# Performance work log

Measured on AMD Instinct MI355X. Metric: run time of the kernel, lower is better.

Reference implementation:

```python
import jax, jax.numpy as jnp
import numpy as np

N = 50000   # nodes
E = 800000  # edges (before self-loops)
IN = 128    # input feature dim
H = 4       # attention heads


def setup_inputs() -> dict:
    key = jax.random.key(0)
    ks = jax.random.split(key, 32)
    f = lambda k, s: (jax.random.normal(k, s, dtype=jnp.float32) * 0.1)
    inp = {
        "x": jax.random.normal(ks[0], (N, IN), dtype=jnp.float32),
        "edge_index": jax.random.randint(ks[1], (2, E), 0, N, dtype=jnp.int32),
        "edge_attr": jax.random.normal(ks[2], (E, 1), dtype=jnp.float32),
        # GATConv 1: 128 -> 8 per head, 4 heads (concat -> 32)
        "W1": f(ks[3], (IN, 32)), "as1": f(ks[4], (H, 8)), "ad1": f(ks[5], (H, 8)), "b1": jnp.zeros((32,), jnp.float32),
        # GATConv 2: 32 -> 16 per head (concat -> 64)
        "W2": f(ks[6], (32, 64)), "as2": f(ks[7], (H, 16)), "ad2": f(ks[8], (H, 16)), "b2": jnp.zeros((64,), jnp.float32),
        # GATConv 3: 64 -> 32 per head (concat -> 128)
        "W3": f(ks[9], (64, 128)), "as3": f(ks[10], (H, 32)), "ad3": f(ks[11], (H, 32)), "b3": jnp.zeros((128,), jnp.float32),
        # GATConv 4: 128 -> 64 per head (concat -> 256)
        "W4": f(ks[12], (128, 256)), "as4": f(ks[13], (H, 64)), "ad4": f(ks[14], (H, 64)), "b4": jnp.zeros((256,), jnp.float32),
        # MLP head
        "Wr": f(ks[15], (256, 32)), "br": jnp.zeros((32,), jnp.float32),
        "Wf1": f(ks[16], (32, 64)), "bf1": jnp.zeros((64,), jnp.float32),
        "Wf2": f(ks[17], (64, 1)), "bf2": jnp.zeros((1,), jnp.float32),
    }
    return inp


def _gat_layer(x, W, a_src, a_dst, bias, src, dst):
    """PyG GATConv (concat=True, negative_slope=0.2, self-loops appended upstream)."""
    heads, C = a_src.shape
    h = (x @ W).reshape(-1, heads, C)              # [N, H, C]
    alpha_s = jnp.sum(h * a_src[None], axis=-1)    # [N, H]
    alpha_d = jnp.sum(h * a_dst[None], axis=-1)    # [N, H]
    e = jax.nn.leaky_relu(alpha_s[src] + alpha_d[dst], 0.2)  # [E', H]
    # segment softmax over incoming edges of each destination node
    emax = jax.ops.segment_max(e, dst, num_segments=N)
    ee = jnp.exp(e - emax[dst])
    denom = jax.ops.segment_sum(ee, dst, num_segments=N)
    alpha = ee / denom[dst]                        # [E', H]
    msg = h[src] * alpha[:, :, None]               # [E', H, C]
    out = jax.ops.segment_sum(msg, dst, num_segments=N)  # [N, H, C]
    return out.reshape(-1, heads * C) + bias


def reference(x, edge_index, edge_attr,
              W1, as1, ad1, b1, W2, as2, ad2, b2,
              W3, as3, ad3, b3, W4, as4, ad4, b4,
              Wr, br, Wf1, bf1, Wf2, bf2):
    # edge_attr is accepted but unused, matching the original forward.
    loop = jnp.arange(N, dtype=edge_index.dtype)
    src = jnp.concatenate([edge_index[0], loop])   # add self-loops (PyG default)
    dst = jnp.concatenate([edge_index[1], loop])
    h = jax.nn.elu(_gat_layer(x, W1, as1, ad1, b1, src, dst))
    h = jax.nn.elu(_gat_layer(h, W2, as2, ad2, b2, src, dst))
    h = jax.nn.elu(_gat_layer(h, W3, as3, ad3, b3, src, dst))
    h = jax.nn.elu(_gat_layer(h, W4, as4, ad4, b4, src, dst))
    h = jax.nn.elu(h @ Wr + br)
    h = jax.nn.elu(h @ Wf1 + bf1)
    return h @ Wf2 + bf2                           # [N, 1]
```

## Files before the change

kernel.cpp:

```cpp
#include <hip/hip_runtime.h>
#include <hip/hip_fp16.h>
#include <math.h>

constexpr int NN = 50000;
constexpr int NE = 800000;
constexpr int NEP = NE + NN;
constexpr int CAP = 96;
constexpr int SCAT_B = (NE / 8 + 255) / 256;
constexpr int PACK_B = 26;
constexpr int NT = (NN + 63) / 64;

typedef _Float16 half8_t __attribute__((ext_vector_type(8)));
typedef float    f32x4_t __attribute__((ext_vector_type(4)));
typedef unsigned int u32x4 __attribute__((ext_vector_type(4)));

__device__ __forceinline__ float lrelu02(float x) { return x > 0.f ? x : 0.2f * x; }
__device__ __forceinline__ float eluf(float x)    { return x > 0.f ? x : (__expf(x) - 1.f); }
__device__ __forceinline__ float pick4(float4 q, int hd) {
  return (hd == 0) ? q.x : (hd == 1) ? q.y : (hd == 2) ? q.z : q.w;
}

#define FMAMIX_LO(accv, pv, uv) \
  asm("v_fma_mix_f32 %0, %1, %2, %0 op_sel:[0,0,0] op_sel_hi:[0,1,0]" \
      : "+v"(accv) : "v"(pv), "v"(uv))
#define FMAMIX_HI(accv, pv, uv) \
  asm("v_fma_mix_f32 %0, %1, %2, %0 op_sel:[0,1,0] op_sel_hi:[0,1,0]" \
      : "+v"(accv) : "v"(pv), "v"(uv))


__device__ __forceinline__ void pack_w_one(const float* __restrict__ W,
                                           __half* __restrict__ Wp,
                                           int M, int tid, int total) {
  if (tid >= total) return;
  int CT = M >> 4;
  int l = tid & 63;
  int c = (tid >> 6) % CT;
  int kc = (tid >> 6) / CT;
  int n = l & 15, q = l >> 4;
  __half* dst = Wp + (size_t)tid * 8;
  const float* src = W + (size_t)(kc * 32 + q * 8) * M + c * 16 + n;
  #pragma unroll
  for (int j = 0; j < 8; j++) dst[j] = __float2half_rn(src[j * M]);
}


template<int M, int C, int CT>
__device__ __forceinline__ void alpha_epilogue(const f32x4_t* acc,
    const float* __restrict__ a_src, const float* __restrict__ a_dst,
    int row_base, int m, float* __restrict__ as_out, float* __restrict__ ad_out) {
  float aS[CT], aD[CT];
  #pragma unroll
  for (int c = 0; c < CT; c++) { aS[c] = a_src[c * 16 + m]; aD[c] = a_dst[c * 16 + m]; }

  if constexpr (C == 8) {
    #pragma unroll
    for (int r = 0; r < 4; r++) {
      float p0 = acc[0][r] * aS[0], p1 = acc[1][r] * aS[1];
      float q0 = acc[0][r] * aD[0], q1 = acc[1][r] * aD[1];
      #pragma unroll
      for (int off = 1; off < 8; off <<= 1) {
        p0 += __shfl_xor(p0, off); p1 += __shfl_xor(p1, off);
        q0 += __shfl_xor(q0, off); q1 += __shfl_xor(q1, off);
      }
      int row = row_base + r;
      if ((m & 7) == 0 && row < NN) {
        int hb = m >> 3;
        as_out[row * 4 + hb]     = p0;
        as_out[row * 4 + 2 + hb] = p1;
        ad_out[row * 4 + hb]     = q0;
        ad_out[row * 4 + 2 + hb] = q1;
      }
    }
  } else {
    constexpr int FPH = C / 16;
    #pragma unroll
    for (int r = 0; r < 4; r++) {
      float bs[4] = {0.f, 0.f, 0.f, 0.f}, bd[4] = {0.f, 0.f, 0.f, 0.f};
      #pragma unroll
      for (int c = 0; c < CT; c++) {
        int hd = c / FPH;
        bs[hd] += acc[c][r] * aS[c];
        bd[hd] += acc[c][r] * aD[c];
      }
      #pragma unroll
      for (int off = 1; off < 16; off <<= 1)
        #pragma unroll
        for (int h = 0; h < 4; h++) {
          bs[h] += __shfl_xor(bs[h], off);
          bd[h] += __shfl_xor(bd[h], off);
        }
      int row = row_base + r;
      if (m < 4 && row < NN) {
        float vs = (m == 0) ? bs[0] : (m == 1) ? bs[1] : (m == 2) ? bs[2] : bs[3];
        float vd = (m == 0) ? bd[0] : (m == 1) ? bd[1] : (m == 2) ? bd[2] : bd[3];
        as_out[row * 4 + m] = vs;
        ad_out[row * 4 + m] = vd;
      }
    }
  }
}


__global__ __launch_bounds__(256) void front_kernel(
    const int* __restrict__ edge_src, const int* __restrict__ edge_dst,
    int* __restrict__ count, int* __restrict__ csr_src,
    const float* __restrict__ W1,
    const float* __restrict__ W2, __half* __restrict__ Wp2,
    const float* __restrict__ W3, __half* __restrict__ Wp3,
    const float* __restrict__ W4, __half* __restrict__ Wp4,
    const float* __restrict__ Wr, __half* __restrict__ Wrp,
    const float* __restrict__ Wf1, __half* __restrict__ Wf1p,
    const float* __restrict__ x, __half* __restrict__ Ch,
    const float* __restrict__ a_src, const float* __restrict__ a_dst,
    float* __restrict__ as_out, float* __restrict__ ad_out) {
  int b = blockIdx.x;
  if (b >= NT) {
    int b2 = b - NT;
    if (b2 < SCAT_B) {
      int e0 = (b2 * 256 + threadIdx.x) * 8;
      if (e0 < NE) {
        int4 sa = *(const int4*)(edge_src + e0);
        int4 sb = *(const int4*)(edge_src + e0 + 4);
        int4 da = *(const int4*)(edge_dst + e0);
        int4 db = *(const int4*)(edge_dst + e0 + 4);
        int p0 = atomicAdd(&count[da.x], 1);
        int p1 = atomicAdd(&count[da.y], 1);
        int p2 = atomicAdd(&count[da.z], 1);
        int p3 = atomicAdd(&count[da.w], 1);
        int p4 = atomicAdd(&count[db.x], 1);
        int p5 = atomicAdd(&count[db.y], 1);
        int p6 = atomicAdd(&count[db.z], 1);
        int p7 = atomicAdd(&count[db.w], 1);
        if (p0 < CAP - 1) csr_src[da.x * CAP + p0] = sa.x;
        if (p1 < CAP - 1) csr_src[da.y * CAP + p1] = sa.y;
        if (p2 < CAP - 1) csr_src[da.z * CAP + p2] = sa.z;
        if (p3 < CAP - 1) csr_src[da.w * CAP + p3] = sa.w;
        if (p4 < CAP - 1) csr_src[db.x * CAP + p4] = sb.x;
        if (p5 < CAP - 1) csr_src[db.y * CAP + p5] = sb.y;
        if (p6 < CAP - 1) csr_src[db.z * CAP + p6] = sb.z;
        if (p7 < CAP - 1) csr_src[db.w * CAP + p7] = sb.w;
      }
      return;
    }
    int tid = (b2 - SCAT_B) * 256 + threadIdx.x;
    if (tid < 256)            pack_w_one(W2, Wp2, 64,  tid,        256);
    else if (tid < 1280)      pack_w_one(W3, Wp3, 128, tid - 256,  1024);
    else if (tid < 5376)      pack_w_one(W4, Wp4, 256, tid - 1280, 4096);
    else if (tid < 6400)      pack_w_one(Wr, Wrp, 32,  tid - 5376, 1024);
    else if (tid < 6656)      pack_w_one(Wf1, Wf1p, 64, tid - 6400, 256);
    return;
  }

  constexpr int M = 32, K = 128, CT = 2, KC = 4;
  __shared__ _Float16 Ah[64 * 40];
  __shared__ _Float16 Bs[KC * CT * 64 * 8];
  int t = threadIdx.x;
  int w = t >> 6, l = t & 63;
  int m = l & 15, q = l >> 4;
  int row0 = b * 64;

  #pragma unroll
  for (int u0 = 0; u0 < 2; u0++) {
    int u = t + u0 * 256;
    int ul = u & 63;
    int uc = (u >> 6) & 1;
    int ukc = u >> 7;
    int un = ul & 15, uq = ul >> 4;
    const float* src = W1 + (size_t)(ukc * 32 + uq * 8) * M + uc * 16 + un;
    _Float16* dst = &Bs[u * 8];
    #pragma unroll
    for (int j = 0; j < 8; j++) dst[j] = (_Float16)src[j * M];
  }

  f32x4_t acc[CT];
  #pragma unroll
  for (int c = 0; c < CT; c++) acc[c] = (f32x4_t){0.f, 0.f, 0.f, 0.f};

  for (int kc = 0; kc < KC; kc++) {
    __syncthreads();
    #pragma unroll
    for (int i = 0; i < 2; i++) {
      int idx = t + 256 * i;
      int row = idx >> 3, c4 = idx & 7;
      int gr = row0 + row; if (gr >= NN) gr = NN - 1;
      float4 v = *(const float4*)(x + (size_t)gr * K + kc * 32 + c4 * 4);
      _Float16 h4[4] = {(_Float16)v.x, (_Float16)v.y, (_Float16)v.z, (_Float16)v.w};
      *(uint2*)(&Ah[row * 40 + c4 * 4]) = *(const uint2*)h4;
    }
    __syncthreads();
    half8_t a = *(const half8_t*)(&Ah[(w * 16 + m) * 40 + q * 8]);
    #pragma unroll
    for (int c = 0; c < CT; c++) {
      half8_t bf = *(const half8_t*)(&Bs[((kc * CT + c) * 64 + l) * 8]);
      acc[c] = __builtin_amdgcn_mfma_f32_16x16x32_f16(a, bf, acc[c], 0, 0, 0);
    }
  }

  #pragma unroll
  for (int r = 0; r < 4; r++) {
    int row = row0 + w * 16 + q * 4 + r;
    if (row < NN) {
      #pragma unroll
      for (int c = 0; c < CT; c++)
        Ch[(size_t)row * M + c * 16 + m] = __float2half_rn(acc[c][r]);
    }
  }
  alpha_epilogue<M, 8, CT>(acc, a_src, a_dst, row0 + w * 16 + q * 4, m, as_out, ad_out);
}


template<int M, int K, int C>
__global__ __launch_bounds__(256) void gemm_mfma_f16_kernel(const __half* __restrict__ A,
    const __half* __restrict__ Wp, __half* __restrict__ Ch,
    const float* __restrict__ a_src, const float* __restrict__ a_dst,
    float* __restrict__ as_out, float* __restrict__ ad_out) {
  constexpr int CT = M / 16;
  constexpr int KC = K / 32;
  __shared__ _Float16 Ah[64 * 40];
  int t = threadIdx.x;
  int w = t >> 6, l = t & 63;
  int m = l & 15, q = l >> 4;
  int row0 = blockIdx.x * 64;

  f32x4_t acc[CT];
  #pragma unroll
  for (int c = 0; c < CT; c++) acc[c] = (f32x4_t){0.f, 0.f, 0.f, 0.f};

  const half8_t* Bfrag = (const half8_t*)Wp;

  for (int kc = 0; kc < KC; kc++) {
    __syncthreads();
    {
      int row = t >> 2, c8 = t & 3;
      int gr = row0 + row; if (gr >= NN) gr = NN - 1;
      uint4 v = *(const uint4*)(A + (size_t)gr * K + kc * 32 + c8 * 8);
      *(uint4*)(&Ah[row * 40 + c8 * 8]) = v;
    }
    __syncthreads();
    half8_t a = *(const half8_t*)(&Ah[(w * 16 + m) * 40 + q * 8]);
    #pragma unroll
    for (int c = 0; c < CT; c++) {
      half8_t b = Bfrag[(kc * CT + c) * 64 + l];
      acc[c] = __builtin_amdgcn_mfma_f32_16x16x32_f16(a, b, acc[c], 0, 0, 0);
    }
  }

  #pragma unroll
  for (int r = 0; r < 4; r++) {
    int row = row0 + w * 16 + q * 4 + r;
    if (row < NN) {
      #pragma unroll
      for (int c = 0; c < CT; c++)
        Ch[(size_t)row * M + c * 16 + m] = __float2half_rn(acc[c][r]);
    }
  }
  alpha_epilogue<M, C, CT>(acc, a_src, a_dst, row0 + w * 16 + q * 4, m, as_out, ad_out);
}


template<int HC, int C>
__global__ __launch_bounds__(256) void agg_kernel(const __half* __restrict__ h,
    const float* __restrict__ as_v, const float* __restrict__ ad_v,
    const int* __restrict__ count, const int* __restrict__ csr_src,
    const float* __restrict__ bias, __half* __restrict__ out) {
  constexpr int V = HC / 8;
  constexpr int G = 64 / V;
  constexpr int D = (HC >= 128) ? 6 : 4;
  __shared__ float4 see4[4][CAP];
  __shared__ int    ssrc[4][CAP];
  int wid = threadIdx.x >> 6, lane = threadIdx.x & 63;
  int dst = blockIdx.x * 4 + wid;
  int base = dst * CAP;
  int degE = count[dst]; if (degE > CAP - 1) degE = CAP - 1;
  int deg = degE + 1;
  float4 ad = *(const float4*)(ad_v + dst * 4);

  float d0 = 0.f, d1 = 0.f, d2 = 0.f, d3 = 0.f;
  #pragma unroll
  for (int it = 0; it < 2; it++) {
    int j = lane + it * 64;
    if (j < deg) {
      int s = (j == 0) ? dst : csr_src[base + j - 1];
      float4 as = *(const float4*)(as_v + s * 4);
      float4 x = make_float4(__expf(lrelu02(as.x + ad.x)), __expf(lrelu02(as.y + ad.y)),
                             __expf(lrelu02(as.z + ad.z)), __expf(lrelu02(as.w + ad.w)));
      ssrc[wid][j] = s; see4[wid][j] = x;
      d0 += x.x; d1 += x.y; d2 += x.z; d3 += x.w;
    }
  }
  #pragma unroll
  for (int off = 32; off > 0; off >>= 1) {
    d0 += __shfl_xor(d0, off); d1 += __shfl_xor(d1, off);
    d2 += __shfl_xor(d2, off); d3 += __shfl_xor(d3, off);
  }
  float4 inv = make_float4(1.f / d0, 1.f / d1, 1.f / d2, 1.f / d3);

  int g = lane / V, v = lane % V;
  int hd = (v * 8) / C;
  float invh = pick4(inv, hd);
  int steps = (deg + G - 1) / G;
  const char* hb = (const char*)h;

  float px[D];
  u32x4 hv[D];

  #define STAGE(kk, jexpr) { \
    int jj = (jexpr) * G + g; \
    bool okk = jj < deg; \
    int jc = okk ? jj : 0; \
    int s = ssrc[wid][jc]; \
    float xx = ((const float*)&see4[wid][jc])[hd]; \
    px[kk] = okk ? xx * invh : 0.f; \
    const void* ap = hb + (size_t)s * (HC * 2) + v * 16; \
    asm volatile("global_load_dwordx4 %0, %1, off" : "=v"(hv[kk]) : "v"(ap) : "memory"); \
  }

  #pragma unroll
  for (int k = 0; k < D; k++) STAGE(k, k)

  float acc[8];
  #pragma unroll
  for (int i = 0; i < 8; i++) acc[i] = 0.f;
  int nB = (steps + D - 1) / D;
  for (int b = 1; b <= nB; b++) {
    #pragma unroll
    for (int k = 0; k < D; k++) {
      if constexpr (D == 6) asm volatile("s_waitcnt vmcnt(5)" ::: "memory");
      else                  asm volatile("s_waitcnt vmcnt(3)" ::: "memory");
      __builtin_amdgcn_sched_barrier(0);
      u32x4 u = hv[k];
      float p = px[k];
      FMAMIX_LO(acc[0], p, u[0]); FMAMIX_HI(acc[1], p, u[0]);
      FMAMIX_LO(acc[2], p, u[1]); FMAMIX_HI(acc[3], p, u[1]);
      FMAMIX_LO(acc[4], p, u[2]); FMAMIX_HI(acc[5], p, u[2]);
      FMAMIX_LO(acc[6], p, u[3]); FMAMIX_HI(acc[7], p, u[3]);
      STAGE(k, b * D + k)
    }
  }
  asm volatile("s_waitcnt vmcnt(0)" ::: "memory");
  __builtin_amdgcn_sched_barrier(0);
  #undef STAGE

  #pragma unroll
  for (int off = V; off < 64; off <<= 1)
    #pragma unroll
    for (int i = 0; i < 8; i++) acc[i] += __shfl_xor(acc[i], off);

  if (lane < V) {
    const float4* b4 = (const float4*)bias;
    float4 ba = b4[2 * v], bb = b4[2 * v + 1];
    _Float16 o[8];
    o[0] = (_Float16)eluf(acc[0] + ba.x); o[1] = (_Float16)eluf(acc[1] + ba.y);
    o[2] = (_Float16)eluf(acc[2] + ba.z); o[3] = (_Float16)eluf(acc[3] + ba.w);
    o[4] = (_Float16)eluf(acc[4] + bb.x); o[5] = (_Float16)eluf(acc[5] + bb.y);
    o[6] = (_Float16)eluf(acc[6] + bb.z); o[7] = (_Float16)eluf(acc[7] + bb.w);
    *(uint4*)(out + (size_t)dst * HC + v * 8) = *(const uint4*)o;
  }
}


__global__ __launch_bounds__(256) void mlp_mfma_kernel(const __half* __restrict__ h4,
    const __half* __restrict__ Wrp, const float* __restrict__ br,
    const __half* __restrict__ Wf1p, const float* __restrict__ bf1,
    const float* __restrict__ Wf2, const float* __restrict__ bf2,
    float* __restrict__ out) {
  __shared__ _Float16 rS[64 * 40];
  int t = threadIdx.x;
  int w = t >> 6, l = t & 63;
  int m = l & 15, q = l >> 4;
  int row0 = blockIdx.x * 64;
  const half8_t* Bwr  = (const half8_t*)Wrp;
  const half8_t* Bwf1 = (const half8_t*)Wf1p;

  int arow = row0 + w * 16 + m; if (arow >= NN) arow = NN - 1;
  const half8_t* Arow = (const half8_t*)(h4 + (size_t)arow * 256);
  half8_t afr[8];
  #pragma unroll
  for (int kc = 0; kc < 8; kc++) afr[kc] = Arow[kc * 4 + q];
  f32x4_t acc1[2];
  acc1[0] = (f32x4_t){0.f, 0.f, 0.f, 0.f};
  acc1[1] = (f32x4_t){0.f, 0.f, 0.f, 0.f};
  #pragma unroll
  for (int kc = 0; kc < 8; kc++) {
    acc1[0] = __builtin_amdgcn_mfma_f32_16x16x32_f16(afr[kc], Bwr[(kc * 2 + 0) * 64 + l], acc1[0], 0, 0, 0);
    acc1[1] = __builtin_amdgcn_mfma_f32_16x16x32_f16(afr[kc], Bwr[(kc * 2 + 1) * 64 + l], acc1[1], 0, 0, 0);
  }
  #pragma unroll
  for (int c = 0; c < 2; c++)
    #pragma unroll
    for (int r = 0; r < 4; r++) {
      float vv = eluf(acc1[c][r] + br[c * 16 + m]);
      rS[(w * 16 + q * 4 + r) * 40 + c * 16 + m] = (_Float16)vv;
    }
  __syncthreads();

  half8_t a2 = *(const half8_t*)(&rS[(w * 16 + m) * 40 + q * 8]);
  f32x4_t acc2[4];
  #pragma unroll
  for (int c = 0; c < 4; c++) acc2[c] = (f32x4_t){0.f, 0.f, 0.f, 0.f};
  #pragma unroll
  for (int c = 0; c < 4; c++)
    acc2[c] = __builtin_amdgcn_mfma_f32_16x16x32_f16(a2, Bwf1[c * 64 + l], acc2[c], 0, 0, 0);

  float wv[4] = {Wf2[m], Wf2[16 + m], Wf2[32 + m], Wf2[48 + m]};
  float rsum[4];
  #pragma unroll
  for (int r = 0; r < 4; r++) {
    float sr = 0.f;
    #pragma unroll
    for (int c = 0; c < 4; c++)
      sr += eluf(acc2[c][r] + bf1[c * 16 + m]) * wv[c];
    #pragma unroll
    for (int off = 1; off < 16; off <<= 1) sr += __shfl_xor(sr, off);
    rsum[r] = sr;
  }
  if (m == 0) {
    float b = bf2[0];
    #pragma unroll
    for (int r = 0; r < 4; r++) {
      int row = row0 + w * 16 + q * 4 + r;
      if (row < NN) out[row] = rsum[r] + b;
    }
  }
}


extern "C" void kernel_launch(void* const* d_in, const int* in_sizes, int n_in,
                              void* d_out, int out_size, void* d_ws, size_t ws_size,
                              hipStream_t stream) {
  const float* x   = (const float*)d_in[0];
  const int*   ei  = (const int*)d_in[1];
  const float* W1  = (const float*)d_in[3];
  const float* as1 = (const float*)d_in[4];
  const float* ad1 = (const float*)d_in[5];
  const float* b1  = (const float*)d_in[6];
  const float* W2  = (const float*)d_in[7];
  const float* as2 = (const float*)d_in[8];
  const float* ad2 = (const float*)d_in[9];
  const float* b2  = (const float*)d_in[10];
  const float* W3  = (const float*)d_in[11];
  const float* as3 = (const float*)d_in[12];
  const float* ad3 = (const float*)d_in[13];
  const float* b3  = (const float*)d_in[14];
  const float* W4  = (const float*)d_in[15];
  const float* as4 = (const float*)d_in[16];
  const float* ad4 = (const float*)d_in[17];
  const float* b4  = (const float*)d_in[18];
  const float* Wr  = (const float*)d_in[19];
  const float* br  = (const float*)d_in[20];
  const float* Wf1 = (const float*)d_in[21];
  const float* bf1 = (const float*)d_in[22];
  const float* Wf2 = (const float*)d_in[23];
  const float* bf2 = (const float*)d_in[24];
  float* out = (float*)d_out;

  char* p = (char*)d_ws;
  auto alloc = [&](size_t bytes) {
    char* q = p;
    p += (bytes + 255) & ~(size_t)255;
    return q;
  };
  int* count   = (int*)alloc((size_t)NN * 4);
  int* csr_src = (int*)alloc((size_t)NN * CAP * 4);
  __half* Hh = (__half*)alloc((size_t)NN * 256 * 2);
  __half* B2 = (__half*)alloc((size_t)NN * 128 * 2);
  __half* B3 = (__half*)alloc((size_t)NN * 256 * 2);
  float* as_buf = (float*)alloc((size_t)NN * 4 * 4);
  float* ad_buf = (float*)alloc((size_t)NN * 4 * 4);
  __half* Wp2 = (__half*)alloc((size_t)32 * 64 * 2);
  __half* Wp3 = (__half*)alloc((size_t)64 * 128 * 2);
  __half* Wp4 = (__half*)alloc((size_t)128 * 256 * 2);
  __half* Wrp = (__half*)alloc((size_t)256 * 32 * 2);
  __half* Wf1p = (__half*)alloc((size_t)32 * 64 * 2);

  const int* edge_src = ei;
  const int* edge_dst = ei + NE;

  hipMemsetAsync(count, 0, (size_t)NN * 4, stream);
  front_kernel<<<NT + SCAT_B + PACK_B, 256, 0, stream>>>(
      edge_src, edge_dst, count, csr_src,
      W1, W2, Wp2, W3, Wp3, W4, Wp4, Wr, Wrp, Wf1, Wf1p,
      x, Hh, as1, ad1, as_buf, ad_buf);

  int gb  = NT;
  int ggb = NN / 4;

  agg_kernel<32, 8><<<ggb, 256, 0, stream>>>(Hh, as_buf, ad_buf, count, csr_src, b1, B2);

  gemm_mfma_f16_kernel<64, 32, 16><<<gb, 256, 0, stream>>>(B2, Wp2, Hh, as2, ad2, as_buf, ad_buf);
  agg_kernel<64, 16><<<ggb, 256, 0, stream>>>(Hh, as_buf, ad_buf, count, csr_src, b2, B3);

  gemm_mfma_f16_kernel<128, 64, 32><<<gb, 256, 0, stream>>>(B3, Wp3, Hh, as3, ad3, as_buf, ad_buf);
  agg_kernel<128, 32><<<ggb, 256, 0, stream>>>(Hh, as_buf, ad_buf, count, csr_src, b3, B2);

  gemm_mfma_f16_kernel<256, 128, 64><<<gb, 256, 0, stream>>>(B2, Wp4, Hh, as4, ad4, as_buf, ad_buf);
  agg_kernel<256, 64><<<ggb, 256, 0, stream>>>(Hh, as_buf, ad_buf, count, csr_src, b4, B3);

  mlp_mfma_kernel<<<gb, 256, 0, stream>>>(B3, Wrp, br, Wf1p, bf1, Wf2, bf2, out);
}
```

Before: 381.6 us.

## Fuse GAT aggregation with next layer's GEMM and attention epilogue

Layers 1-3 now use one fused kernel per layer. Each 512-thread block aggregates 64 destination nodes (8 per wave), keeps the ELU'd result in shared memory, then multiplies it by the next weight matrix with MFMA and computes the next layer's attention coefficients. This removes the global write and reload of the intermediate activations and three kernel launches. The cost is fewer blocks (782 instead of 12500), each with serial per-wave work, so occupancy and load balance for the latency-bound gather may suffer. Ping-pong buffers are added for the features and attention scores.

```diff
diff --git a/kernel.cpp b/kernel.cpp
--- a/kernel.cpp
+++ b/kernel.cpp
@@ -4,10 +4,8 @@
 
 constexpr int NN = 50000;
 constexpr int NE = 800000;
-constexpr int NEP = NE + NN;
 constexpr int CAP = 96;
 constexpr int SCAT_B = (NE / 8 + 255) / 256;
-constexpr int PACK_B = 26;
 constexpr int NT = (NN + 63) / 64;
 
 typedef _Float16 half8_t __attribute__((ext_vector_type(8)));
@@ -26,6 +24,17 @@
 #define FMAMIX_HI(accv, pv, uv) \
   asm("v_fma_mix_f32 %0, %1, %2, %0 op_sel:[0,1,0] op_sel_hi:[0,1,0]" \
       : "+v"(accv) : "v"(pv), "v"(uv))
+
+#define STAGE_G(kk, jexpr, STRIDE) { \
+    int jj = (jexpr) * G + g; \
+    bool okk = jj < deg; \
+    int jc = okk ? jj : 0; \
+    int s = ssrc[wid][jc]; \
+    float xx = ((const float*)&see4[wid][jc])[hd]; \
+    px[kk] = okk ? xx * invh : 0.f; \
+    const void* ap = hb + (size_t)s * (STRIDE) + v * 16; \
+    asm volatile("global_load_dwordx4 %0, %1, off" : "=v"(hv[kk]) : "v"(ap) : "memory"); \
+  }
 
 
 __device__ __forceinline__ void pack_w_one(const float* __restrict__ W,
@@ -44,58 +53,28 @@
 }
 
 
-template<int M, int C, int CT>
-__device__ __forceinline__ void alpha_epilogue(const f32x4_t* acc,
+__device__ __forceinline__ void alpha_epilogue8(const f32x4_t* acc,
     const float* __restrict__ a_src, const float* __restrict__ a_dst,
     int row_base, int m, float* __restrict__ as_out, float* __restrict__ ad_out) {
-  float aS[CT], aD[CT];
-  #pragma unroll
-  for (int c = 0; c < CT; c++) { aS[c] = a_src[c * 16 + m]; aD[c] = a_dst[c * 16 + m]; }
-
-  if constexpr (C == 8) {
-    #pragma unroll
-    for (int r = 0; r < 4; r++) {
-      float p0 = acc[0][r] * aS[0], p1 = acc[1][r] * aS[1];
-      float q0 = acc[0][r] * aD[0], q1 = acc[1][r] * aD[1];
-      #pragma unroll
-      for (int off = 1; off < 8; off <<= 1) {
-        p0 += __shfl_xor(p0, off); p1 += __shfl_xor(p1, off);
-        q0 += __shfl_xor(q0, off); q1 += __shfl_xor(q1, off);
-      }
-      int row = row_base + r;
-      if ((m & 7) == 0 && row < NN) {
-        int hb = m >> 3;
-        as_out[row * 4 + hb]     = p0;
-        as_out[row * 4 + 2 + hb] = p1;
-        ad_out[row * 4 + hb]     = q0;
-        ad_out[row * 4 + 2 + hb] = q1;
-      }
-    }
-  } else {
-    constexpr int FPH = C / 16;
-    #pragma unroll
-    for (int r = 0; r < 4; r++) {
-      float bs[4] = {0.f, 0.f, 0.f, 0.f}, bd[4] = {0.f, 0.f, 0.f, 0.f};
-      #pragma unroll
-      for (int c = 0; c < CT; c++) {
-        int hd = c / FPH;
-        bs[hd] += acc[c][r] * aS[c];
-        bd[hd] += acc[c][r] * aD[c];
-      }
-      #pragma unroll
-      for (int off = 1; off < 16; off <<= 1)
-        #pragma unroll
-        for (int h = 0; h < 4; h++) {
-          bs[h] += __shfl_xor(bs[h], off);
-          bd[h] += __shfl_xor(bd[h], off);
-        }
-      int row = row_base + r;
-      if (m < 4 && row < NN) {
-        float vs = (m == 0) ? bs[0] : (m == 1) ? bs[1] : (m == 2) ? bs[2] : bs[3];
-        float vd = (m == 0) ? bd[0] : (m == 1) ? bd[1] : (m == 2) ? bd[2] : bd[3];
-        as_out[row * 4 + m] = vs;
-        ad_out[row * 4 + m] = vd;
-      }
+  float aS[2], aD[2];
+  #pragma unroll
+  for (int c = 0; c < 2; c++) { aS[c] = a_src[c * 16 + m]; aD[c] = a_dst[c * 16 + m]; }
+  #pragma unroll
+  for (int r = 0; r < 4; r++) {
+    float p0 = acc[0][r] * aS[0], p1 = acc[1][r] * aS[1];
+    float q0 = acc[0][r] * aD[0], q1 = acc[1][r] * aD[1];
+    #pragma unroll
+    for (int off = 1; off < 8; off <<= 1) {
+      p0 += __shfl_xor(p0, off); p1 += __shfl_xor(p1, off);
+      q0 += __shfl_xor(q0, off); q1 += __shfl_xor(q1, off);
+    }
+    int row = row_base + r;
+    if ((m & 7) == 0 && row < NN) {
+      int hb2 = m >> 3;
+      as_out[row * 4 + hb2]     = p0;
+      as_out[row * 4 + 2 + hb2] = p1;
+      ad_out[row * 4 + hb2]     = q0;
+      ad_out[row * 4 + 2 + hb2] = q1;
     }
   }
 }
@@ -183,8 +162,8 @@
       int idx = t + 256 * i;
       int row = idx >> 3, c4 = idx & 7;
       int gr = row0 + row; if (gr >= NN) gr = NN - 1;
-      float4 v = *(const float4*)(x + (size_t)gr * K + kc * 32 + c4 * 4);
-      _Float16 h4[4] = {(_Float16)v.x, (_Float16)v.y, (_Float16)v.z, (_Float16)v.w};
+      float4 vv = *(const float4*)(x + (size_t)gr * K + kc * 32 + c4 * 4);
+      _Float16 h4[4] = {(_Float16)vv.x, (_Float16)vv.y, (_Float16)vv.z, (_Float16)vv.w};
       *(uint2*)(&Ah[row * 40 + c4 * 4]) = *(const uint2*)h4;
     }
     __syncthreads();
@@ -205,56 +184,172 @@
         Ch[(size_t)row * M + c * 16 + m] = __float2half_rn(acc[c][r]);
     }
   }
-  alpha_epilogue<M, 8, CT>(acc, a_src, a_dst, row0 + w * 16 + q * 4, m, as_out, ad_out);
-}
-
-
-template<int M, int K, int C>
-__global__ __launch_bounds__(256) void gemm_mfma_f16_kernel(const __half* __restrict__ A,
-    const __half* __restrict__ Wp, __half* __restrict__ Ch,
-    const float* __restrict__ a_src, const float* __restrict__ a_dst,
+  alpha_epilogue8(acc, a_src, a_dst, row0 + w * 16 + q * 4, m, as_out, ad_out);
+}
+
+
+template<int MK, int KK, int CC>
+__global__ __launch_bounds__(512) void fused_agg_gemm_kernel(
+    const __half* __restrict__ hin,
+    const float* __restrict__ as_v, const float* __restrict__ ad_v,
+    const int* __restrict__ count, const int* __restrict__ csr_src,
+    const float* __restrict__ bias,
+    const __half* __restrict__ Wp,
+    __half* __restrict__ hout,
+    const float* __restrict__ a_src2, const float* __restrict__ a_dst2,
     float* __restrict__ as_out, float* __restrict__ ad_out) {
-  constexpr int CT = M / 16;
-  constexpr int KC = K / 32;
-  __shared__ _Float16 Ah[64 * 40];
+  constexpr int V = KK / 8;
+  constexpr int G = 64 / V;
+  constexpr int D = (KK >= 128) ? 6 : 4;
+  constexpr int CIN = KK / 4;
+  constexpr int CT = MK / 16;
+  constexpr int CTH = CT / 2;
+  constexpr int KC = KK / 32;
+  constexpr int LDA = KK + 8;
+  __shared__ float4 see4[8][CAP];
+  __shared__ int    ssrc[8][CAP];
+  __shared__ _Float16 As[64 * LDA];
   int t = threadIdx.x;
-  int w = t >> 6, l = t & 63;
-  int m = l & 15, q = l >> 4;
+  int wid = t >> 6, lane = t & 63;
   int row0 = blockIdx.x * 64;
 
-  f32x4_t acc[CT];
-  #pragma unroll
-  for (int c = 0; c < CT; c++) acc[c] = (f32x4_t){0.f, 0.f, 0.f, 0.f};
-
-  const half8_t* Bfrag = (const half8_t*)Wp;
-
+  int g = lane / V, v = lane % V;
+  int hd = (v * 8) / CIN;
+  const char* hb = (const char*)hin;
+
+  #pragma unroll 1
+  for (int dq = 0; dq < 8; dq++) {
+    int dst0 = row0 + wid * 8 + dq;
+    int dst = dst0 < NN ? dst0 : NN - 1;
+    int base = dst * CAP;
+    int degE = count[dst]; if (degE > CAP - 1) degE = CAP - 1;
+    int deg = degE + 1;
+    float4 ad = *(const float4*)(ad_v + dst * 4);
+
+    float d0 = 0.f, d1 = 0.f, d2 = 0.f, d3 = 0.f;
+    #pragma unroll
+    for (int it = 0; it < 2; it++) {
+      int j = lane + it * 64;
+      if (j < deg) {
+        int s = (j == 0) ? dst : csr_src[base + j - 1];
+        float4 as = *(const float4*)(as_v + s * 4);
+        float4 xv = make_float4(__expf(lrelu02(as.x + ad.x)), __expf(lrelu02(as.y + ad.y)),
+                                __expf(lrelu02(as.z + ad.z)), __expf(lrelu02(as.w + ad.w)));
+        ssrc[wid][j] = s; see4[wid][j] = xv;
+        d0 += xv.x; d1 += xv.y; d2 += xv.z; d3 += xv.w;
+      }
+    }
+    #pragma unroll
+    for (int off = 32; off > 0; off >>= 1) {
+      d0 += __shfl_xor(d0, off); d1 += __shfl_xor(d1, off);
+      d2 += __shfl_xor(d2, off); d3 += __shfl_xor(d3, off);
+    }
+    float4 inv = make_float4(1.f / d0, 1.f / d1, 1.f / d2, 1.f / d3);
+    float invh = pick4(inv, hd);
+    int steps = (deg + G - 1) / G;
+
+    float px[D];
+    u32x4 hv[D];
+    #pragma unroll
+    for (int k = 0; k < D; k++) STAGE_G(k, k, KK * 2)
+
+    float acc[8];
+    #pragma unroll
+    for (int i = 0; i < 8; i++) acc[i] = 0.f;
+    int nB = (steps + D - 1) / D;
+    for (int bb = 1; bb <= nB; bb++) {
+      #pragma unroll
+      for (int k = 0; k < D; k++) {
+        if constexpr (D == 6) asm volatile("s_waitcnt vmcnt(5)" ::: "memory");
+        else                  asm volatile("s_waitcnt vmcnt(3)" ::: "memory");
+        __builtin_amdgcn_sched_barrier(0);
+        u32x4 u = hv[k];
+        float p = px[k];
+        FMAMIX_LO(acc[0], p, u[0]); FMAMIX_HI(acc[1], p, u[0]);
+        FMAMIX_LO(acc[2], p, u[1]); FMAMIX_HI(acc[3], p, u[1]);
+        FMAMIX_LO(acc[4], p, u[2]); FMAMIX_HI(acc[5], p, u[2]);
+        FMAMIX_LO(acc[6], p, u[3]); FMAMIX_HI(acc[7], p, u[3]);
+        STAGE_G(k, bb * D + k, KK * 2)
+      }
+    }
+    asm volatile("s_waitcnt vmcnt(0)" ::: "memory");
+    __builtin_amdgcn_sched_barrier(0);
+
+    #pragma unroll
+    for (int off = V; off < 64; off <<= 1)
+      #pragma unroll
+      for (int i = 0; i < 8; i++) acc[i] += __shfl_xor(acc[i], off);
+
+    if (lane < V) {
+      const float4* b4 = (const float4*)bias;
+      float4 ba = b4[2 * v], bbv = b4[2 * v + 1];
+      _Float16 o[8];
+      o[0] = (_Float16)eluf(acc[0] + ba.x);  o[1] = (_Float16)eluf(acc[1] + ba.y);
+      o[2] = (_Float16)eluf(acc[2] + ba.z);  o[3] = (_Float16)eluf(acc[3] + ba.w);
+      o[4] = (_Float16)eluf(acc[4] + bbv.x); o[5] = (_Float16)eluf(acc[5] + bbv.y);
+      o[6] = (_Float16)eluf(acc[6] + bbv.z); o[7] = (_Float16)eluf(acc[7] + bbv.w);
+      *(uint4*)(&As[(wid * 8 + dq) * LDA + v * 8]) = *(const uint4*)o;
+    }
+  }
+  __syncthreads();
+
+  int wr = wid & 3, wc = wid >> 2;
+  int m = lane & 15, q = lane >> 4;
+  f32x4_t gacc[CTH];
+  #pragma unroll
+  for (int cl = 0; cl < CTH; cl++) gacc[cl] = (f32x4_t){0.f, 0.f, 0.f, 0.f};
+  const half8_t* Bf = (const half8_t*)Wp;
+  #pragma unroll
   for (int kc = 0; kc < KC; kc++) {
-    __syncthreads();
-    {
-      int row = t >> 2, c8 = t & 3;
-      int gr = row0 + row; if (gr >= NN) gr = NN - 1;
-      uint4 v = *(const uint4*)(A + (size_t)gr * K + kc * 32 + c8 * 8);
-      *(uint4*)(&Ah[row * 40 + c8 * 8]) = v;
-    }
-    __syncthreads();
-    half8_t a = *(const half8_t*)(&Ah[(w * 16 + m) * 40 + q * 8]);
-    #pragma unroll
-    for (int c = 0; c < CT; c++) {
-      half8_t b = Bfrag[(kc * CT + c) * 64 + l];
-      acc[c] = __builtin_amdgcn_mfma_f32_16x16x32_f16(a, b, acc[c], 0, 0, 0);
+    half8_t a = *(const half8_t*)(&As[(wr * 16 + m) * LDA + kc * 32 + q * 8]);
+    #pragma unroll
+    for (int cl = 0; cl < CTH; cl++) {
+      int c = wc * CTH + cl;
+      gacc[cl] = __builtin_amdgcn_mfma_f32_16x16x32_f16(a, Bf[(kc * CT + c) * 64 + lane], gacc[cl], 0, 0, 0);
     }
   }
 
   #pragma unroll
   for (int r = 0; r < 4; r++) {
-    int row = row0 + w * 16 + q * 4 + r;
+    int row = row0 + wr * 16 + q * 4 + r;
     if (row < NN) {
       #pragma unroll
-      for (int c = 0; c < CT; c++)
-        Ch[(size_t)row * M + c * 16 + m] = __float2half_rn(acc[c][r]);
-    }
-  }
-  alpha_epilogue<M, C, CT>(acc, a_src, a_dst, row0 + w * 16 + q * 4, m, as_out, ad_out);
+      for (int cl = 0; cl < CTH; cl++)
+        hout[(size_t)row * MK + (wc * CTH + cl) * 16 + m] = __float2half_rn(gacc[cl][r]);
+    }
+  }
+
+  constexpr int FPH = CC / 16;
+  float aS[CTH], aD[CTH];
+  #pragma unroll
+  for (int cl = 0; cl < CTH; cl++) {
+    int c = wc * CTH + cl;
+    aS[cl] = a_src2[c * 16 + m];
+    aD[cl] = a_dst2[c * 16 + m];
+  }
+  #pragma unroll
+  for (int r = 0; r < 4; r++) {
+    float bs[2] = {0.f, 0.f}, bd[2] = {0.f, 0.f};
+    #pragma unroll
+    for (int cl = 0; cl < CTH; cl++) {
+      int c = wc * CTH + cl;
+      int hl = c / FPH - wc * 2;
+      bs[hl] += gacc[cl][r] * aS[cl];
+      bd[hl] += gacc[cl][r] * aD[cl];
+    }
+    #pragma unroll
+    for (int off = 1; off < 16; off <<= 1) {
+      bs[0] += __shfl_xor(bs[0], off); bs[1] += __shfl_xor(bs[1], off);
+      bd[0] += __shfl_xor(bd[0], off); bd[1] += __shfl_xor(bd[1], off);
+    }
+    int row = row0 + wr * 16 + q * 4 + r;
+    if ((m >> 1) == wc && row < NN) {
+      float vs = (m & 1) ? bs[1] : bs[0];
+      float vd = (m & 1) ? bd[1] : bd[0];
+      as_out[row * 4 + m] = vs;
+      ad_out[row * 4 + m] = vd;
+    }
+  }
 }
 
 
@@ -282,10 +377,10 @@
     if (j < deg) {
       int s = (j == 0) ? dst : csr_src[base + j - 1];
       float4 as = *(const float4*)(as_v + s * 4);
-      float4 x = make_float4(__expf(lrelu02(as.x + ad.x)), __expf(lrelu02(as.y + ad.y)),
-                             __expf(lrelu02(as.z + ad.z)), __expf(lrelu02(as.w + ad.w)));
-      ssrc[wid][j] = s; see4[wid][j] = x;
-      d0 += x.x; d1 += x.y; d2 += x.z; d3 += x.w;
+      float4 xv = make_float4(__expf(lrelu02(as.x + ad.x)), __expf(lrelu02(as.y + ad.y)),
+                              __expf(lrelu02(as.z + ad.z)), __expf(lrelu02(as.w + ad.w)));
+      ssrc[wid][j] = s; see4[wid][j] = xv;
+      d0 += xv.x; d1 += xv.y; d2 += xv.z; d3 += xv.w;
     }
   }
   #pragma unroll
@@ -303,20 +398,8 @@
 
   float px[D];
   u32x4 hv[D];
-
-  #define STAGE(kk, jexpr) { \
-    int jj = (jexpr) * G + g; \
-    bool okk = jj < deg; \
-    int jc = okk ? jj : 0; \
-    int s = ssrc[wid][jc]; \
-    float xx = ((const float*)&see4[wid][jc])[hd]; \
-    px[kk] = okk ? xx * invh : 0.f; \
-    const void* ap = hb + (size_t)s * (HC * 2) + v * 16; \
-    asm volatile("global_load_dwordx4 %0, %1, off" : "=v"(hv[kk]) : "v"(ap) : "memory"); \
-  }
-
-  #pragma unroll
-  for (int k = 0; k < D; k++) STAGE(k, k)
+  #pragma unroll
+  for (int k = 0; k < D; k++) STAGE_G(k, k, HC * 2)
 
   float acc[8];
   #pragma unroll
@@ -334,12 +417,11 @@
       FMAMIX_LO(acc[2], p, u[1]); FMAMIX_HI(acc[3], p, u[1]);
       FMAMIX_LO(acc[4], p, u[2]); FMAMIX_HI(acc[5], p, u[2]);
       FMAMIX_LO(acc[6], p, u[3]); FMAMIX_HI(acc[7], p, u[3]);
-      STAGE(k, b * D + k)
+      STAGE_G(k, b * D + k, HC * 2)
     }
   }
   asm volatile("s_waitcnt vmcnt(0)" ::: "memory");
   __builtin_amdgcn_sched_barrier(0);
-  #undef STAGE
 
   #pragma unroll
   for (int off = V; off < 64; off <<= 1)
@@ -462,11 +544,12 @@
   };
   int* count   = (int*)alloc((size_t)NN * 4);
   int* csr_src = (int*)alloc((size_t)NN * CAP * 4);
-  __half* Hh = (__half*)alloc((size_t)NN * 256 * 2);
-  __half* B2 = (__half*)alloc((size_t)NN * 128 * 2);
-  __half* B3 = (__half*)alloc((size_t)NN * 256 * 2);
-  float* as_buf = (float*)alloc((size_t)NN * 4 * 4);
-  float* ad_buf = (float*)alloc((size_t)NN * 4 * 4);
+  __half* HhA = (__half*)alloc((size_t)NN * 256 * 2);
+  __half* HhB = (__half*)alloc((size_t)NN * 256 * 2);
+  float* asA = (float*)alloc((size_t)NN * 4 * 4);
+  float* adA = (float*)alloc((size_t)NN * 4 * 4);
+  float* asB = (float*)alloc((size_t)NN * 4 * 4);
+  float* adB = (float*)alloc((size_t)NN * 4 * 4);
   __half* Wp2 = (__half*)alloc((size_t)32 * 64 * 2);
   __half* Wp3 = (__half*)alloc((size_t)64 * 128 * 2);
   __half* Wp4 = (__half*)alloc((size_t)128 * 256 * 2);
@@ -477,24 +560,18 @@
   const int* edge_dst = ei + NE;
 
   hipMemsetAsync(count, 0, (size_t)NN * 4, stream);
-  front_kernel<<<NT + SCAT_B + PACK_B, 256, 0, stream>>>(
+  front_kernel<<<NT + SCAT_B + 26, 256, 0, stream>>>(
       edge_src, edge_dst, count, csr_src,
       W1, W2, Wp2, W3, Wp3, W4, Wp4, Wr, Wrp, Wf1, Wf1p,
-      x, Hh, as1, ad1, as_buf, ad_buf);
-
-  int gb  = NT;
-  int ggb = NN / 4;
-
-  agg_kernel<32, 8><<<ggb, 256, 0, stream>>>(Hh, as_buf, ad_buf, count, csr_src, b1, B2);
-
-  gemm_mfma_f16_kernel<64, 32, 16><<<gb, 256, 0, stream>>>(B2, Wp2, Hh, as2, ad2, as_buf, ad_buf);
-  agg_kernel<64, 16><<<ggb, 256, 0, stream>>>(Hh, as_buf, ad_buf, count, csr_src, b2, B3);
-
-  gemm_mfma_f16_kernel<128, 64, 32><<<gb, 256, 0, stream>>>(B3, Wp3, Hh, as3, ad3, as_buf, ad_buf);
-  agg_kernel<128, 32><<<ggb, 256, 0, stream>>>(Hh, as_buf, ad_buf, count, csr_src, b3, B2);
-
-  gemm_mfma_f16_kernel<256, 128, 64><<<gb, 256, 0, stream>>>(B2, Wp4, Hh, as4, ad4, as_buf, ad_buf);
-  agg_kernel<256, 64><<<ggb, 256, 0, stream>>>(Hh, as_buf, ad_buf, count, csr_src, b4, B3);
-
-  mlp_mfma_kernel<<<gb, 256, 0, stream>>>(B3, Wrp, br, Wf1p, bf1, Wf2, bf2, out);
-}
+      x, HhA, as1, ad1, asA, adA);
+
+  fused_agg_gemm_kernel<64, 32, 16><<<NT, 512, 0, stream>>>(
+      HhA, asA, adA, count, csr_src, b1, Wp2, HhB, as2, ad2, asB, adB);
+  fused_agg_gemm_kernel<128, 64, 32><<<NT, 512, 0, stream>>>(
+      HhB, asB, adB, count, csr_src, b2, Wp3, HhA, as3, ad3, asA, adA);
+  fused_agg_gemm_kernel<256, 128, 64><<<NT, 512, 0, stream>>>(
+      HhA, asA, adA, count, csr_src, b3, Wp4, HhB, as4, ad4, asB, adB);
+
+  agg_kernel<256, 64><<<NN / 4, 256, 0, stream>>>(HhB, asB, adB, count, csr_src, b4, HhA);
+  mlp_mfma_kernel<<<NT, 256, 0, stream>>>(HhA, Wrp, br, Wf1p, bf1, Wf2, bf2, out);
+}
```

New measurement: 414.0 us. +8.5%, slower.
